# Performance work log

Measured on AMD Instinct MI355X. Metric: run time of the kernel, lower is better.

Reference implementation:

```python
import jax, jax.numpy as jnp
import numpy as np

B, N, ENC, DEC, ATT = 32, 4096, 1024, 512, 512


def setup_inputs() -> dict:
    key = jax.random.key(0)
    ks = jax.random.split(key, 8)
    s_enc = 1.0 / np.sqrt(ENC)
    s_dec = 1.0 / np.sqrt(DEC)
    s_att = 1.0 / np.sqrt(ATT)
    return {
        "encoder_out": jax.random.normal(ks[0], (B, N, ENC), jnp.float32),
        "decoder_hidden": jax.random.normal(ks[1], (B, DEC), jnp.float32),
        "W_enc": jax.random.uniform(ks[2], (ENC, ATT), jnp.float32, -s_enc, s_enc),
        "b_enc": jax.random.uniform(ks[3], (ATT,), jnp.float32, -s_enc, s_enc),
        "W_dec": jax.random.uniform(ks[4], (DEC, ATT), jnp.float32, -s_dec, s_dec),
        "b_dec": jax.random.uniform(ks[5], (ATT,), jnp.float32, -s_dec, s_dec),
        "w_full": jax.random.uniform(ks[6], (ATT,), jnp.float32, -s_att, s_att),
        "b_full": jax.random.uniform(ks[7], (), jnp.float32, -s_att, s_att),
    }


def reference(encoder_out, decoder_hidden, W_enc, b_enc, W_dec, b_dec, w_full, b_full):
    # att1: [B, N, ATT]; att2: [B, 1, ATT]
    att1 = jnp.einsum('bne,ea->bna', encoder_out, W_enc) + b_enc
    att2 = (decoder_hidden @ W_dec + b_dec)[:, None, :]
    att = jax.nn.relu(att1 + att2)
    e = jnp.einsum('bna,a->bn', att, w_full) + b_full  # [B, N]
    alpha = jax.nn.softmax(e, axis=1)
    awe = jnp.einsum('bne,bn->be', encoder_out, alpha)  # weighted encoding [B, ENC]
    return awe, alpha
```

## Files before the change

### kernel.cpp

```cpp
#include <hip/hip_runtime.h>

#define B_ 32
#define N_ 4096
#define ENC_ 1024
#define DEC_ 512
#define ATT_ 512

typedef __attribute__((ext_vector_type(8))) short short8;
typedef __attribute__((ext_vector_type(4))) short short4v;
typedef __attribute__((ext_vector_type(4))) float f32x4;

__device__ __forceinline__ short f2bf(float f) {
  union { float f; unsigned u; } x; x.f = f;
  unsigned r = (x.u + 0x7FFFu + ((x.u >> 16) & 1u)) >> 16;
  return (short)r;
}

__device__ __forceinline__ void lds_barrier() {
  asm volatile("s_waitcnt lgkmcnt(0)" ::: "memory");
  __builtin_amdgcn_s_barrier();
  asm volatile("" ::: "memory");
}

extern "C" __global__ void __launch_bounds__(256) prep_kernel(
    const float* __restrict__ dh, const float* __restrict__ W_dec,
    const float* __restrict__ b_dec, const float* __restrict__ b_enc,
    const float* __restrict__ W_enc,
    float* __restrict__ att2, short* __restrict__ Wfrag)
{
  if (blockIdx.x < B_) {
    __shared__ float dhs[DEC_];
    int b = blockIdx.x;
    for (int i = threadIdx.x; i < DEC_; i += 256) dhs[i] = dh[b * DEC_ + i];
    __syncthreads();
    for (int a = threadIdx.x; a < ATT_; a += 256) {
      float s = b_dec[a] + b_enc[a];
      for (int k = 0; k < DEC_; ++k) s += dhs[k] * W_dec[k * ATT_ + a];
      att2[b * ATT_ + a] = s;
    }
  } else {
    int idx = (blockIdx.x - B_) * 256 + threadIdx.x;
    int l = idx & 63;
    int t = (idx >> 6) & 31;
    int c = idx >> 11;
    int col = c * 16 + (l & 15);
    int kb = t * 32 + (l >> 4) * 8;
    short8 p;
#pragma unroll
    for (int j = 0; j < 8; ++j) p[j] = f2bf(W_enc[(kb + j) * ATT_ + col]);
    *(short8*)(Wfrag + ((long)idx << 3)) = p;
  }
}

extern "C" __global__ void __launch_bounds__(512, 4) gemm_e_kernel(
    const float* __restrict__ enc, const short* __restrict__ Wfrag,
    const float* __restrict__ att2, const float* __restrict__ w_full,
    float* __restrict__ e_out)
{
  __shared__ __align__(16) short As[2][64 * 32];
  __shared__ float e_red[64][8];

  const int tid = threadIdx.x;
  const int lane = tid & 63;
  const int w = tid >> 6;
  const int blk = blockIdx.x;
  const int b = blk >> 6;
  const int n0 = (blk & 63) * 64;

  const int arow = tid >> 3;
  const int akc = tid & 7;
  const float* aptr = enc + ((long)(b * N_ + n0 + arow)) * ENC_ + akc * 4;
  const int awbyte = (arow * 64 + akc * 8) ^ ((arow & 7) << 4);

  int arbyte[4];
#pragma unroll
  for (int r = 0; r < 4; ++r) {
    int rr = r * 16 + (lane & 15);
    arbyte[r] = (rr * 64 + ((lane >> 4) * 16)) ^ ((rr & 7) << 4);
  }

  const short* bbase = Wfrag + (long)(w * 4) * 32 * 512 + lane * 8;

  f32x4 acc[4][4] = {};

  {
    f32x4 p0 = *(const f32x4*)(aptr);
    short4v q;
#pragma unroll
    for (int j = 0; j < 4; ++j) q[j] = f2bf(p0[j]);
    *(short4v*)((char*)(&As[0][0]) + awbyte) = q;
  }
  f32x4 pA = *(const f32x4*)(aptr + 32);
  lds_barrier();

#pragma unroll 2
  for (int t = 0; t < 32; ++t) {
    const int cur = t & 1;
    f32x4 pB;
    if (t + 2 < 32) pB = *(const f32x4*)(aptr + (t + 2) * 32);

    short8 bfg[4];
#pragma unroll
    for (int c = 0; c < 4; ++c)
      bfg[c] = *(const short8*)(bbase + c * 16384 + t * 512);

    short8 af[4];
#pragma unroll
    for (int r = 0; r < 4; ++r)
      af[r] = *(const short8*)((const char*)(&As[cur][0]) + arbyte[r]);

#pragma unroll
    for (int c = 0; c < 4; ++c)
#pragma unroll
      for (int r = 0; r < 4; ++r)
        acc[r][c] = __builtin_amdgcn_mfma_f32_16x16x32_bf16(af[r], bfg[c],
                                                            acc[r][c], 0, 0, 0);

    if (t + 1 < 32) {
      short4v q;
#pragma unroll
      for (int j = 0; j < 4; ++j) q[j] = f2bf(pA[j]);
      *(short4v*)((char*)(&As[cur ^ 1][0]) + awbyte) = q;
    }
    pA = pB;
    lds_barrier();
  }

  const int lq = lane >> 4, lr = lane & 15;
  float at2v[4], wv[4];
#pragma unroll
  for (int c = 0; c < 4; ++c) {
    int col = w * 64 + c * 16 + lr;
    at2v[c] = att2[b * ATT_ + col];
    wv[c] = w_full[col];
  }
#pragma unroll
  for (int r = 0; r < 4; ++r) {
#pragma unroll
    for (int j = 0; j < 4; ++j) {
      float s = 0.f;
#pragma unroll
      for (int c = 0; c < 4; ++c)
        s += fmaxf(acc[r][c][j] + at2v[c], 0.f) * wv[c];
      s += __shfl_xor(s, 1); s += __shfl_xor(s, 2);
      s += __shfl_xor(s, 4); s += __shfl_xor(s, 8);
      if (lr == 0) e_red[r * 16 + lq * 4 + j][w] = s;
    }
  }
  __syncthreads();
  if (tid < 64) {
    float ev = 0.f;
#pragma unroll
    for (int ww = 0; ww < 8; ++ww) ev += e_red[tid][ww];
    e_out[b * N_ + n0 + tid] = ev;
  }
}

extern "C" __global__ void __launch_bounds__(256) softmax_kernel(
    const float* __restrict__ e, float* __restrict__ alpha)
{
  int b = blockIdx.x, tid = threadIdx.x;
  float v[16];
  float m = -1e30f;
#pragma unroll
  for (int i = 0; i < 16; ++i) {
    v[i] = e[b * N_ + i * 256 + tid];
    m = fmaxf(m, v[i]);
  }
  for (int off = 1; off < 64; off <<= 1) m = fmaxf(m, __shfl_xor(m, off));
  __shared__ float redm[4];
  if ((tid & 63) == 0) redm[tid >> 6] = m;
  __syncthreads();
  m = fmaxf(fmaxf(redm[0], redm[1]), fmaxf(redm[2], redm[3]));
  float s = 0.f;
#pragma unroll
  for (int i = 0; i < 16; ++i) { v[i] = expf(v[i] - m); s += v[i]; }
  for (int off = 1; off < 64; off <<= 1) s += __shfl_xor(s, off);
  __shared__ float reds[4];
  if ((tid & 63) == 0) reds[tid >> 6] = s;
  __syncthreads();
  s = reds[0] + reds[1] + reds[2] + reds[3];
  float inv = 1.0f / s;
#pragma unroll
  for (int i = 0; i < 16; ++i) alpha[b * N_ + i * 256 + tid] = v[i] * inv;
}

extern "C" __global__ void __launch_bounds__(256) awe_part_kernel(
    const float* __restrict__ enc, const float* __restrict__ alpha,
    float* __restrict__ part)
{
  __shared__ float als[256];
  __shared__ f32x4 red[256];
  int bi = blockIdx.x;
  int b = bi & 31, cchunk = (bi >> 5) & 3, nchunk = bi >> 7;
  int t = threadIdx.x;
  int n0 = nchunk * 256;
  als[t] = alpha[b * N_ + n0 + t];
  __syncthreads();
  int tcol = t & 63, tn = t >> 6;
  const float* base = enc + (long)b * N_ * ENC_ + (long)n0 * ENC_ +
                      cchunk * 256 + tcol * 4;
  f32x4 acc = {};
  for (int i = tn; i < 256; i += 4) {
    f32x4 vv = *(const f32x4*)(base + (long)i * ENC_);
    acc += als[i] * vv;
  }
  red[t] = acc;
  __syncthreads();
  if (t < 64) {
    f32x4 s = red[t] + red[t + 64] + red[t + 128] + red[t + 192];
    *(f32x4*)(&part[(long)nchunk * 32768 + b * 1024 + cchunk * 256 + t * 4]) = s;
  }
}

extern "C" __global__ void __launch_bounds__(256) awe_reduce_kernel(
    const float* __restrict__ part, float* __restrict__ awe)
{
  int i = blockIdx.x * 256 + threadIdx.x;
  float s = 0.f;
#pragma unroll
  for (int p = 0; p < 16; ++p) s += part[(long)p * 32768 + i];
  awe[i] = s;
}

extern "C" void kernel_launch(void* const* d_in, const int* in_sizes, int n_in,
                              void* d_out, int out_size, void* d_ws, size_t ws_size,
                              hipStream_t stream) {
  const float* enc    = (const float*)d_in[0];
  const float* dh     = (const float*)d_in[1];
  const float* W_enc  = (const float*)d_in[2];
  const float* b_enc  = (const float*)d_in[3];
  const float* W_dec  = (const float*)d_in[4];
  const float* b_dec  = (const float*)d_in[5];
  const float* w_full = (const float*)d_in[6];
  float* out = (float*)d_out;

  char* ws = (char*)d_ws;
  float* att2  = (float*)ws;
  short* Wfrag = (short*)(ws + 65536);
  float* e_buf = (float*)(ws + 65536 + 1048576);
  float* part  = (float*)(ws + 65536 + 1048576 + 524288);

  hipLaunchKernelGGL(prep_kernel, dim3(B_ + 256), dim3(256), 0, stream,
                     dh, W_dec, b_dec, b_enc, W_enc, att2, Wfrag);
  hipLaunchKernelGGL(gemm_e_kernel, dim3(2048), dim3(512), 0, stream,
                     enc, Wfrag, att2, w_full, e_buf);
  hipLaunchKernelGGL(softmax_kernel, dim3(B_), dim3(256), 0, stream,
                     e_buf, out + B_ * ENC_);
  hipLaunchKernelGGL(awe_part_kernel, dim3(2048), dim3(256), 0, stream,
                     enc, out + B_ * ENC_, part);
  hipLaunchKernelGGL(awe_reduce_kernel, dim3(128), dim3(256), 0, stream,
                     part, out);
}
```

Measured before the change: 331.8 us.

## Double K-tile to 64 and prefetch B fragments one step ahead in GEMM

The encoder GEMM main loop now processes 64-wide K slices per iteration (16 iterations instead of 32), halving the barrier count. The loop double-buffers the W fragments in registers, loading the next step's fragments before the MFMAs, and raises wave priority around the MFMA block with s_setprio. The occupancy hint of 4 in launch_bounds is removed. This raises register pressure and LDS use, which may lower occupancy.

```diff
diff --git a/kernel.cpp b/kernel.cpp
--- a/kernel.cpp
+++ b/kernel.cpp
@@ -5,9 +5,9 @@
 #define ENC_ 1024
 #define DEC_ 512
 #define ATT_ 512
+#define NT_ 16
 
 typedef __attribute__((ext_vector_type(8))) short short8;
-typedef __attribute__((ext_vector_type(4))) short short4v;
 typedef __attribute__((ext_vector_type(4))) float f32x4;
 
 __device__ __forceinline__ short f2bf(float f) {
@@ -52,12 +52,12 @@
   }
 }
 
-extern "C" __global__ void __launch_bounds__(512, 4) gemm_e_kernel(
+extern "C" __global__ void __launch_bounds__(512) gemm_e_kernel(
     const float* __restrict__ enc, const short* __restrict__ Wfrag,
     const float* __restrict__ att2, const float* __restrict__ w_full,
     float* __restrict__ e_out)
 {
-  __shared__ __align__(16) short As[2][64 * 32];
+  __shared__ __align__(16) short As[2][64 * 64];
   __shared__ float e_red[64][8];
 
   const int tid = threadIdx.x;
@@ -69,62 +69,91 @@
 
   const int arow = tid >> 3;
   const int akc = tid & 7;
-  const float* aptr = enc + ((long)(b * N_ + n0 + arow)) * ENC_ + akc * 4;
-  const int awbyte = (arow * 64 + akc * 8) ^ ((arow & 7) << 4);
-
-  int arbyte[4];
+  const float* aptr = enc + ((long)(b * N_ + n0 + arow)) * ENC_ + akc * 8;
+  const int awbyte = (arow * 128 + akc * 16) ^ ((arow & 7) << 4);
+
+  int arbyte[4][2];
 #pragma unroll
   for (int r = 0; r < 4; ++r) {
     int rr = r * 16 + (lane & 15);
-    arbyte[r] = (rr * 64 + ((lane >> 4) * 16)) ^ ((rr & 7) << 4);
-  }
-
-  const short* bbase = Wfrag + (long)(w * 4) * 32 * 512 + lane * 8;
+#pragma unroll
+    for (int kk = 0; kk < 2; ++kk)
+      arbyte[r][kk] = (rr * 128 + (lane >> 4) * 16 + kk * 64) ^ ((rr & 7) << 4);
+  }
+
+  const short* bptr = Wfrag + (long)(w * 4) * 16384 + lane * 8;
 
   f32x4 acc[4][4] = {};
+  short8 bfg[2][2][4];
+  f32x4 pAB[2][2];
 
   {
-    f32x4 p0 = *(const f32x4*)(aptr);
-    short4v q;
-#pragma unroll
-    for (int j = 0; j < 4; ++j) q[j] = f2bf(p0[j]);
-    *(short4v*)((char*)(&As[0][0]) + awbyte) = q;
-  }
-  f32x4 pA = *(const f32x4*)(aptr + 32);
+    f32x4 a0 = *(const f32x4*)(aptr);
+    f32x4 a1 = *(const f32x4*)(aptr + 4);
+    short8 q;
+#pragma unroll
+    for (int j = 0; j < 4; ++j) { q[j] = f2bf(a0[j]); q[j + 4] = f2bf(a1[j]); }
+    *(short8*)((char*)(&As[0][0]) + awbyte) = q;
+  }
+#pragma unroll
+  for (int cc = 0; cc < 4; ++cc) {
+    bfg[0][0][cc] = *(const short8*)(bptr + cc * 16384 + 0 * 512);
+    bfg[0][1][cc] = *(const short8*)(bptr + cc * 16384 + 1 * 512);
+  }
+  pAB[0][0] = *(const f32x4*)(aptr + 64);
+  pAB[0][1] = *(const f32x4*)(aptr + 64 + 4);
   lds_barrier();
 
-#pragma unroll 2
-  for (int t = 0; t < 32; ++t) {
-    const int cur = t & 1;
-    f32x4 pB;
-    if (t + 2 < 32) pB = *(const f32x4*)(aptr + (t + 2) * 32);
-
-    short8 bfg[4];
-#pragma unroll
-    for (int c = 0; c < 4; ++c)
-      bfg[c] = *(const short8*)(bbase + c * 16384 + t * 512);
-
-    short8 af[4];
-#pragma unroll
-    for (int r = 0; r < 4; ++r)
-      af[r] = *(const short8*)((const char*)(&As[cur][0]) + arbyte[r]);
-
-#pragma unroll
-    for (int c = 0; c < 4; ++c)
-#pragma unroll
-      for (int r = 0; r < 4; ++r)
-        acc[r][c] = __builtin_amdgcn_mfma_f32_16x16x32_bf16(af[r], bfg[c],
-                                                            acc[r][c], 0, 0, 0);
-
-    if (t + 1 < 32) {
-      short4v q;
-#pragma unroll
-      for (int j = 0; j < 4; ++j) q[j] = f2bf(pA[j]);
-      *(short4v*)((char*)(&As[cur ^ 1][0]) + awbyte) = q;
-    }
-    pA = pB;
-    lds_barrier();
-  }
+#define GSTEP(CUR, NXT, T)                                                    \
+  {                                                                           \
+    if ((T) + 1 < NT_) {                                                      \
+      _Pragma("unroll")                                                       \
+      for (int cc = 0; cc < 4; ++cc) {                                        \
+        bfg[NXT][0][cc] =                                                     \
+            *(const short8*)(bptr + cc * 16384 + (2 * ((T) + 1)) * 512);      \
+        bfg[NXT][1][cc] =                                                     \
+            *(const short8*)(bptr + cc * 16384 + (2 * ((T) + 1) + 1) * 512);  \
+      }                                                                       \
+    }                                                                         \
+    if ((T) + 2 < NT_) {                                                      \
+      pAB[NXT][0] = *(const f32x4*)(aptr + ((T) + 2) * 64);                   \
+      pAB[NXT][1] = *(const f32x4*)(aptr + ((T) + 2) * 64 + 4);               \
+    }                                                                         \
+    short8 af[2][4];                                                          \
+    _Pragma("unroll")                                                         \
+    for (int r = 0; r < 4; ++r) {                                             \
+      af[0][r] = *(const short8*)((const char*)(&As[CUR][0]) + arbyte[r][0]); \
+      af[1][r] = *(const short8*)((const char*)(&As[CUR][0]) + arbyte[r][1]); \
+    }                                                                         \
+    __builtin_amdgcn_s_setprio(1);                                            \
+    _Pragma("unroll")                                                         \
+    for (int cc = 0; cc < 4; ++cc) {                                          \
+      _Pragma("unroll")                                                       \
+      for (int r = 0; r < 4; ++r) {                                           \
+        acc[r][cc] = __builtin_amdgcn_mfma_f32_16x16x32_bf16(                 \
+            af[0][r], bfg[CUR][0][cc], acc[r][cc], 0, 0, 0);                  \
+        acc[r][cc] = __builtin_amdgcn_mfma_f32_16x16x32_bf16(                 \
+            af[1][r], bfg[CUR][1][cc], acc[r][cc], 0, 0, 0);                  \
+      }                                                                       \
+    }                                                                         \
+    __builtin_amdgcn_s_setprio(0);                                            \
+    if ((T) + 1 < NT_) {                                                      \
+      short8 q;                                                               \
+      _Pragma("unroll")                                                       \
+      for (int j = 0; j < 4; ++j) {                                           \
+        q[j] = f2bf(pAB[CUR][0][j]);                                          \
+        q[j + 4] = f2bf(pAB[CUR][1][j]);                                      \
+      }                                                                       \
+      *(short8*)((char*)(&As[NXT][0]) + awbyte) = q;                          \
+    }                                                                         \
+    lds_barrier();                                                            \
+  }
+
+  for (int tt = 0; tt < NT_; tt += 2) {
+    GSTEP(0, 1, tt);
+    GSTEP(1, 0, tt + 1);
+  }
+#undef GSTEP
 
   const int lq = lane >> 4, lr = lane & 15;
   float at2v[4], wv[4];
```

Result: slower. 352.5 us (+6.2%).

## Widen GEMM K-tile to 128 with register double-buffered B fragments

Applied to the files above, without the earlier changes.

The fused GEMM+score kernel now stages 128-wide K slices of the encoder tile in LDS instead of 32, so there are 8 barriers per tile rather than 32. Each thread loads 16 floats per stage. B fragments are prefetched one sub-step ahead into alternating register sets, and s_setprio wraps the MFMA bursts. Dropping the occupancy hint from launch bounds and quadrupling LDS per block may lower the number of resident blocks and raise register pressure.

```diff
diff --git a/kernel.cpp b/kernel.cpp
--- a/kernel.cpp
+++ b/kernel.cpp
@@ -7,7 +7,6 @@
 #define ATT_ 512
 
 typedef __attribute__((ext_vector_type(8))) short short8;
-typedef __attribute__((ext_vector_type(4))) short short4v;
 typedef __attribute__((ext_vector_type(4))) float f32x4;
 
 __device__ __forceinline__ short f2bf(float f) {
@@ -41,10 +40,10 @@
   } else {
     int idx = (blockIdx.x - B_) * 256 + threadIdx.x;
     int l = idx & 63;
-    int t = (idx >> 6) & 31;
+    int g = (idx >> 6) & 31;
     int c = idx >> 11;
     int col = c * 16 + (l & 15);
-    int kb = t * 32 + (l >> 4) * 8;
+    int kb = g * 32 + (l >> 4) * 8;
     short8 p;
 #pragma unroll
     for (int j = 0; j < 8; ++j) p[j] = f2bf(W_enc[(kb + j) * ATT_ + col]);
@@ -52,12 +51,12 @@
   }
 }
 
-extern "C" __global__ void __launch_bounds__(512, 4) gemm_e_kernel(
+extern "C" __global__ void __launch_bounds__(512) gemm_e_kernel(
     const float* __restrict__ enc, const short* __restrict__ Wfrag,
     const float* __restrict__ att2, const float* __restrict__ w_full,
     float* __restrict__ e_out)
 {
-  __shared__ __align__(16) short As[2][64 * 32];
+  __shared__ __align__(16) short As[2][64 * 128];
   __shared__ float e_red[64][8];
 
   const int tid = threadIdx.x;
@@ -69,61 +68,92 @@
 
   const int arow = tid >> 3;
   const int akc = tid & 7;
-  const float* aptr = enc + ((long)(b * N_ + n0 + arow)) * ENC_ + akc * 4;
-  const int awbyte = (arow * 64 + akc * 8) ^ ((arow & 7) << 4);
-
-  int arbyte[4];
+  const float* aptr = enc + ((long)(b * N_ + n0 + arow)) * ENC_ + akc * 16;
+  const int awb0 = (arow * 256 + akc * 32) ^ ((arow & 7) << 4);
+  const int awb1 = (arow * 256 + akc * 32 + 16) ^ ((arow & 7) << 4);
+
+  int Pb[4], amask[4];
 #pragma unroll
   for (int r = 0; r < 4; ++r) {
     int rr = r * 16 + (lane & 15);
-    arbyte[r] = (rr * 64 + ((lane >> 4) * 16)) ^ ((rr & 7) << 4);
-  }
-
-  const short* bbase = Wfrag + (long)(w * 4) * 32 * 512 + lane * 8;
+    Pb[r] = rr * 256 + (lane >> 4) * 16;
+    amask[r] = (rr & 7) << 4;
+  }
+
+  const short* bptr = Wfrag + (long)(w * 4) * 16384 + lane * 8;
 
   f32x4 acc[4][4] = {};
+  short8 bfgA[4], bfgB[4];
+  f32x4 pA[4];
 
   {
-    f32x4 p0 = *(const f32x4*)(aptr);
-    short4v q;
-#pragma unroll
-    for (int j = 0; j < 4; ++j) q[j] = f2bf(p0[j]);
-    *(short4v*)((char*)(&As[0][0]) + awbyte) = q;
-  }
-  f32x4 pA = *(const f32x4*)(aptr + 32);
+    f32x4 v0 = *(const f32x4*)(aptr);
+    f32x4 v1 = *(const f32x4*)(aptr + 4);
+    f32x4 v2 = *(const f32x4*)(aptr + 8);
+    f32x4 v3 = *(const f32x4*)(aptr + 12);
+    short8 q0, q1;
+#pragma unroll
+    for (int j = 0; j < 4; ++j) {
+      q0[j] = f2bf(v0[j]); q0[j + 4] = f2bf(v1[j]);
+      q1[j] = f2bf(v2[j]); q1[j + 4] = f2bf(v3[j]);
+    }
+    *(short8*)((char*)As[0] + awb0) = q0;
+    *(short8*)((char*)As[0] + awb1) = q1;
+  }
+#pragma unroll
+  for (int cc = 0; cc < 4; ++cc)
+    bfgA[cc] = *(const short8*)(bptr + cc * 16384);
   lds_barrier();
 
-#pragma unroll 2
-  for (int t = 0; t < 32; ++t) {
+#pragma unroll
+  for (int t = 0; t < 8; ++t) {
     const int cur = t & 1;
-    f32x4 pB;
-    if (t + 2 < 32) pB = *(const f32x4*)(aptr + (t + 2) * 32);
-
-    short8 bfg[4];
-#pragma unroll
-    for (int c = 0; c < 4; ++c)
-      bfg[c] = *(const short8*)(bbase + c * 16384 + t * 512);
-
-    short8 af[4];
-#pragma unroll
-    for (int r = 0; r < 4; ++r)
-      af[r] = *(const short8*)((const char*)(&As[cur][0]) + arbyte[r]);
-
-#pragma unroll
-    for (int c = 0; c < 4; ++c)
+    if (t + 1 < 8) {
+#pragma unroll
+      for (int i = 0; i < 4; ++i)
+        pA[i] = *(const f32x4*)(aptr + (t + 1) * 128 + i * 4);
+    }
+#pragma unroll
+    for (int s = 0; s < 4; ++s) {
+      const int g = t * 4 + s;
+      if (g + 1 < 32) {
+        if ((s & 1) == 0) {
+#pragma unroll
+          for (int cc = 0; cc < 4; ++cc)
+            bfgB[cc] = *(const short8*)(bptr + cc * 16384 + (g + 1) * 512);
+        } else {
+#pragma unroll
+          for (int cc = 0; cc < 4; ++cc)
+            bfgA[cc] = *(const short8*)(bptr + cc * 16384 + (g + 1) * 512);
+        }
+      }
+      short8 af[4];
 #pragma unroll
       for (int r = 0; r < 4; ++r)
-        acc[r][c] = __builtin_amdgcn_mfma_f32_16x16x32_bf16(af[r], bfg[c],
-                                                            acc[r][c], 0, 0, 0);
-
-    if (t + 1 < 32) {
-      short4v q;
-#pragma unroll
-      for (int j = 0; j < 4; ++j) q[j] = f2bf(pA[j]);
-      *(short4v*)((char*)(&As[cur ^ 1][0]) + awbyte) = q;
-    }
-    pA = pB;
-    lds_barrier();
+        af[r] = *(const short8*)((const char*)As[cur] +
+                                 ((Pb[r] + s * 64) ^ amask[r]));
+      __builtin_amdgcn_s_setprio(1);
+#pragma unroll
+      for (int cc = 0; cc < 4; ++cc) {
+#pragma unroll
+        for (int r = 0; r < 4; ++r)
+          acc[r][cc] = __builtin_amdgcn_mfma_f32_16x16x32_bf16(
+              af[r], ((s & 1) == 0) ? bfgA[cc] : bfgB[cc], acc[r][cc],
+              0, 0, 0);
+      }
+      __builtin_amdgcn_s_setprio(0);
+    }
+    if (t + 1 < 8) {
+      short8 q0, q1;
+#pragma unroll
+      for (int j = 0; j < 4; ++j) {
+        q0[j] = f2bf(pA[0][j]); q0[j + 4] = f2bf(pA[1][j]);
+        q1[j] = f2bf(pA[2][j]); q1[j + 4] = f2bf(pA[3][j]);
+      }
+      *(short8*)((char*)As[cur ^ 1] + awb0) = q0;
+      *(short8*)((char*)As[cur ^ 1] + awb1) = q1;
+      lds_barrier();
+    }
   }
 
   const int lq = lane >> 4, lr = lane & 15;
```

After: 332.3 us. Within noise of the previous version (+0.1%).
